# Performance work log

Measured on AMD Instinct MI355X. Metric: run time of the kernel, lower is better.

## Reference

```python
import jax, jax.numpy as jnp
import numpy as np

B, Q, C, H, N, D, F = 1, 2048, 2048, 1024, 16, 64, 4096
R = Q + C  # relative position encoding length
EPS = 1e-12
NEG = 1e30


def setup_inputs() -> dict:
    key = jax.random.key(0)
    ks = jax.random.split(key, 16)
    s = 0.02
    return dict(
        content_stream=jax.random.normal(ks[0], (B, Q, H), jnp.float32),
        content_mask=jnp.zeros((B, 1, Q, C), jnp.float32),
        context=jax.random.normal(ks[1], (B, C, H), jnp.float32),
        position_encoding=jax.random.normal(ks[2], (B, R, H), jnp.float32),
        content_bias=jax.random.normal(ks[3], (N, D), jnp.float32) * s,
        position_bias=jax.random.normal(ks[4], (N, D), jnp.float32) * s,
        segment_encoding=jax.random.normal(ks[5], (2, N, D), jnp.float32) * s,
        segment_matrix=jax.random.randint(ks[6], (B, Q, C), 0, 2).astype(bool),
        segment_bias=jax.random.normal(ks[7], (N, D), jnp.float32) * s,
        Wq=jax.random.normal(ks[8], (H, N, D), jnp.float32) * s,
        Wk=jax.random.normal(ks[9], (H, N, D), jnp.float32) * s,
        Wv=jax.random.normal(ks[10], (H, N, D), jnp.float32) * s,
        Wr=jax.random.normal(ks[11], (H, N, D), jnp.float32) * s,
        Wo=jax.random.normal(ks[12], (H, N, D), jnp.float32) * s,
        ln1_gamma=jnp.ones((H,), jnp.float32),
        ln1_beta=jnp.zeros((H,), jnp.float32),
        W1=jax.random.normal(ks[13], (H, F), jnp.float32) * s,
        b1=jnp.zeros((F,), jnp.float32),
        W2=jax.random.normal(ks[14], (F, H), jnp.float32) * s,
        b2=jnp.zeros((H,), jnp.float32),
        ln2_gamma=jnp.ones((H,), jnp.float32),
        ln2_beta=jnp.zeros((H,), jnp.float32),
    )


def _layernorm(x, g, b):
    m = jnp.mean(x, axis=-1, keepdims=True)
    v = jnp.mean(jnp.square(x - m), axis=-1, keepdims=True)
    return (x - m) * jax.lax.rsqrt(v + EPS) * g + b


def _rel_shift(x, klen):
    # x: [b, n, q, r] -> shifted [b, n, q, klen] (XLNet reshape trick)
    b, n, q, r = x.shape
    x = x.reshape(b, n, r, q)[:, :, 1:, :].reshape(b, n, q, r - 1)
    return x[:, :, :, :klen]


def reference(content_stream, content_mask, context, position_encoding,
              content_bias, position_bias, segment_encoding, segment_matrix,
              segment_bias, Wq, Wk, Wv, Wr, Wo, ln1_gamma, ln1_beta,
              W1, b1, W2, b2, ln2_gamma, ln2_beta):
    q = jnp.einsum('bqh,hnd->bqnd', content_stream, Wq)
    k = jnp.einsum('bch,hnd->bcnd', context, Wk)
    v = jnp.einsum('bch,hnd->bcnd', context, Wv)
    r = jnp.einsum('brh,hnd->brnd', position_encoding, Wr)

    # content / position / segment bias terms (XLNet relative attention)
    ac = jnp.einsum('bqnd,bcnd->bnqc', q + content_bias, k)
    bd = _rel_shift(jnp.einsum('bqnd,brnd->bnqr', q + position_bias, r),
                    k.shape[1])
    ef = jnp.einsum('bqnd,snd->bnqs', q + segment_bias, segment_encoding)
    ef = jnp.where(segment_matrix[:, None], ef[..., 1:], ef[..., :1])

    scores = (ac + bd + ef) / jnp.sqrt(jnp.float32(D))
    scores = scores - NEG * content_mask  # mask: 1.0 = disallowed
    probs = jax.nn.softmax(scores, axis=-1)

    attn = jnp.einsum('bnqc,bcnd->bqnd', probs, v)
    attn_out = jnp.einsum('bqnd,hnd->bqh', attn, Wo)

    # residual + LN, then FFN, residual + LN (dropout off: training=False)
    ffn_in = _layernorm(attn_out + content_stream, ln1_gamma, ln1_beta)
    ffn_out = jax.nn.relu(ffn_in @ W1 + b1) @ W2 + b2
    return _layernorm(ffn_out + ffn_in, ln2_gamma, ln2_beta)
```

## Files before the change

### kernel.cpp

```cpp
#include <hip/hip_runtime.h>
#include <stdint.h>


typedef unsigned short ushort_t;
typedef __attribute__((ext_vector_type(8))) short bf16x8;
typedef __attribute__((ext_vector_type(4))) float f32x4;

#define QLEN 2048
#define CLEN 2048
#define HDIM 1024
#define NHEAD 16
#define DHEAD 64
#define RLEN 4096
#define FDIM 4096

__device__ __forceinline__ float bf2f(ushort_t u) {
  union { float f; uint32_t i; } x; x.i = ((uint32_t)u) << 16; return x.f;
}
__device__ __forceinline__ ushort_t f2bf(float f) {
  union { float f; uint32_t i; } x; x.f = f;
  uint32_t r = x.i + 0x7fffu + ((x.i >> 16) & 1u);
  return (ushort_t)(r >> 16);
}
__device__ __forceinline__ f32x4 mfma16(bf16x8 a, bf16x8 b, f32x4 c) {
  return __builtin_amdgcn_mfma_f32_16x16x32_bf16(a, b, c, 0, 0, 0);
}
__device__ __forceinline__ bool probe_bf16(const uint32_t* probe) {
  return probe[0] == 0x3F803F80u;
}

typedef const __attribute__((address_space(1))) void* gas_t;
typedef __attribute__((address_space(3))) void* las_t;
__device__ __forceinline__ void glds16(const void* g, void* l) {
  __builtin_amdgcn_global_load_lds((gas_t)(uintptr_t)g, (las_t)(uintptr_t)l, 16, 0, 0);
}

__device__ __forceinline__ void bar_lds() {
  __asm__ volatile("s_waitcnt lgkmcnt(0)\n\ts_barrier" ::: "memory");
}
__device__ __forceinline__ void bar_full() {
  __asm__ volatile("s_waitcnt vmcnt(0) lgkmcnt(0)\n\ts_barrier" ::: "memory");
}

struct ConvJobs {
  const void* src[5];
  const void* mask_src;
  ushort_t* dst[5];
  int n[5];
  int blk0[6];
};

__global__ __launch_bounds__(256) void conv_all(
    ConvJobs J, const uint32_t* __restrict__ probe)
{
  const bool isb = probe_bf16(probe);
  int j = 0;
  #pragma unroll
  for (int t = 1; t < 5; t++) if ((int)blockIdx.x >= J.blk0[t]) j = t;
  const int lb = blockIdx.x - J.blk0[j];
  const int nb = J.blk0[j + 1] - J.blk0[j];
  const int n = J.n[j];
  ushort_t* dst = J.dst[j];
  if (j < 4) {
    const void* src = J.src[j];
    for (int i = lb * 256 + threadIdx.x; i < n; i += nb * 256)
      dst[i] = isb ? ((const ushort_t*)src)[i] : f2bf(((const float*)src)[i]);
  } else {
    const void* sm = J.src[4];
    uint32_t sw = 0;
    #pragma unroll
    for (int t = 0; t < 8; t++) sw |= ((const uint32_t*)sm)[t];
    const bool i8 = sw > 1u;
    for (int i = lb * 256 + threadIdx.x; i < n; i += nb * 256) {
      const int s = i8 ? (int)((const unsigned char*)sm)[i]
                       : (int)((const uint32_t*)sm)[i];
      const float mv = isb ? bf2f(((const ushort_t*)J.mask_src)[i])
                           : ((const float*)J.mask_src)[i];
      const float f = (float)(s ? 1 : 0) + (mv != 0.f ? 2.f : 0.f);
      dst[i] = f2bf(f);
    }
  }
}

struct SmallBatch {
  const void* src[10];
  int n[10];
  int off[10];
};

__global__ __launch_bounds__(256) void convert_small(
    SmallBatch sb, ushort_t* __restrict__ dst, const uint32_t* __restrict__ probe)
{
  const bool isb = probe_bf16(probe);
  const int t = blockIdx.x;
  const void* s = sb.src[t];
  ushort_t* d = dst + sb.off[t];
  for (int i = threadIdx.x; i < sb.n[t]; i += 256)
    d[i] = isb ? ((const ushort_t*)s)[i] : f2bf(((const float*)s)[i]);
}

struct TransJobs { const void* src[4]; ushort_t* dst[4]; };
__global__ __launch_bounds__(256) void transpose4_to_bf16(
    TransJobs T, int R, int C, const uint32_t* __restrict__ probe)
{
  const bool isb = probe_bf16(probe);
  const void* in = T.src[blockIdx.z];
  ushort_t* out = T.dst[blockIdx.z];
  __shared__ ushort_t t[32][33];
  const int bx = blockIdx.x * 32, by = blockIdx.y * 32;
  const int x = threadIdx.x & 31, y0 = threadIdx.x >> 5;
  #pragma unroll
  for (int yy = 0; yy < 32; yy += 8) {
    const size_t idx = (size_t)(by + y0 + yy) * C + bx + x;
    t[y0 + yy][x] = isb ? ((const ushort_t*)in)[idx] : f2bf(((const float*)in)[idx]);
  }
  __syncthreads();
  #pragma unroll
  for (int yy = 0; yy < 32; yy += 8)
    out[(size_t)(bx + y0 + yy) * R + by + x] = t[x][y0 + yy];
}

__global__ __launch_bounds__(256) void transpose_to_bf16(
    const void* __restrict__ in, ushort_t* __restrict__ out, int R, int C,
    const uint32_t* __restrict__ probe)
{
  const bool isb = probe_bf16(probe);
  __shared__ ushort_t t[32][33];
  const int bx = blockIdx.x * 32, by = blockIdx.y * 32;
  const int x = threadIdx.x & 31, y0 = threadIdx.x >> 5;
  #pragma unroll
  for (int yy = 0; yy < 32; yy += 8) {
    const size_t idx = (size_t)(by + y0 + yy) * C + bx + x;
    t[y0 + yy][x] = isb ? ((const ushort_t*)in)[idx] : f2bf(((const float*)in)[idx]);
  }
  __syncthreads();
  #pragma unroll
  for (int yy = 0; yy < 32; yy += 8)
    out[(size_t)(bx + y0 + yy) * R + by + x] = t[x][y0 + yy];
}

__device__ __forceinline__ void gemm_store(
    void* out, const ushort_t* bias, int M, int N, int epi,
    int gm, int gn, float v)
{
  if (epi == 0) {
    ((ushort_t*)out)[(size_t)gm * N + gn] = f2bf(v);
  } else if (epi == 1) {
    ((ushort_t*)out)[(size_t)gn * M + gm] = f2bf(v);
  } else if (epi == 2) {
    ((float*)out)[(size_t)gm * N + gn] = v;
  } else if (epi == 3) {
    v += bf2f(bias[gn]); v = v > 0.f ? v : 0.f;
    ((ushort_t*)out)[(size_t)gm * N + gn] = f2bf(v);
  } else if (epi == 4) {
    v += bf2f(bias[gn]);
    ((float*)out)[(size_t)gm * N + gn] = v;
  } else if (epi == 5) {
    ((ushort_t*)out)[((size_t)(gn >> 6) * M + gm) * 64 + (gn & 63)] = f2bf(v);
  } else {
    if (gn < 1024)
      ((ushort_t*)out)[((size_t)(gn >> 6) * M + gm) * 64 + (gn & 63)] = f2bf(v);
    else
      ((ushort_t*)out)[(size_t)2097152 + (size_t)(gn - 1024) * M + gm] = f2bf(v);
  }
}

__global__ __launch_bounds__(256) void gemm_bt_kernel(
    const ushort_t* __restrict__ A, const ushort_t* __restrict__ Bt,
    const ushort_t* __restrict__ bias, void* __restrict__ out,
    int M, int N, int K, int epi)
{
  __shared__ __attribute__((aligned(16))) ushort_t As[2][128 * 32];
  __shared__ __attribute__((aligned(16))) ushort_t Bs[2][64 * 32];
  const int tid = threadIdx.x;
  const int lane = tid & 63, wave = tid >> 6;
  const int l15 = lane & 15, quad = lane >> 4;
  const int m0 = blockIdx.y * 128, n0 = blockIdx.x * 64;

  const int arow = tid >> 2;
  const int acol = (tid & 3) * 8;

  f32x4 acc[2][4];
  #pragma unroll
  for (int i = 0; i < 2; i++)
    #pragma unroll
    for (int j = 0; j < 4; j++) acc[i][j] = (f32x4){0.f, 0.f, 0.f, 0.f};

  const int KI = K >> 5;
  glds16(&A[(size_t)(m0 + arow) * K + acol], &As[0][tid * 8]);
  glds16(&A[(size_t)(m0 + arow + 64) * K + acol], &As[0][tid * 8 + 2048]);
  glds16(&Bt[(size_t)(n0 + arow) * K + acol], &Bs[0][tid * 8]);
  bar_full();

  for (int ki = 0; ki < KI; ki++) {
    const int b = ki & 1;
    if (ki + 1 < KI) {
      const int k1 = (ki + 1) << 5;
      glds16(&A[(size_t)(m0 + arow) * K + k1 + acol], &As[b ^ 1][tid * 8]);
      glds16(&A[(size_t)(m0 + arow + 64) * K + k1 + acol], &As[b ^ 1][tid * 8 + 2048]);
      glds16(&Bt[(size_t)(n0 + arow) * K + k1 + acol], &Bs[b ^ 1][tid * 8]);
    }
    bf16x8 af[2], bfr[4];
    #pragma unroll
    for (int i = 0; i < 2; i++)
      af[i] = *(const bf16x8*)&As[b][(wave * 32 + i * 16 + l15) * 32 + quad * 8];
    #pragma unroll
    for (int j = 0; j < 4; j++)
      bfr[j] = *(const bf16x8*)&Bs[b][(j * 16 + l15) * 32 + quad * 8];
    #pragma unroll
    for (int i = 0; i < 2; i++)
      #pragma unroll
      for (int j = 0; j < 4; j++)
        acc[i][j] = mfma16(af[i], bfr[j], acc[i][j]);
    bar_full();
  }

  #pragma unroll
  for (int i = 0; i < 2; i++)
    #pragma unroll
    for (int j = 0; j < 4; j++)
      #pragma unroll
      for (int rg = 0; rg < 4; rg++)
        gemm_store(out, bias, M, N, epi,
                   m0 + wave * 32 + i * 16 + quad * 4 + rg,
                   n0 + j * 16 + l15, acc[i][j][rg]);
}

struct Ptr4 { void* p[4]; };
__global__ __launch_bounds__(256) void gemm128_bt_kernel(
    const ushort_t* __restrict__ A, const ushort_t* __restrict__ Bt,
    const ushort_t* __restrict__ bias, Ptr4 outs,
    int M, int N, int K, int Kc, int epi)
{
  __shared__ __attribute__((aligned(16))) ushort_t As[2][128 * 32];
  __shared__ __attribute__((aligned(16))) ushort_t Bs[2][128 * 32];
  const int tid = threadIdx.x;
  const int lane = tid & 63, wave = tid >> 6;
  const int l15 = lane & 15, quad = lane >> 4;
  const int wm = wave >> 1, wn = wave & 1;
  const int m0 = blockIdx.y * 128, n0 = blockIdx.x * 128;
  const int kb = blockIdx.z * Kc;
  void* out = outs.p[blockIdx.z];

  const int arow = tid >> 2;
  const int acol = (tid & 3) * 8;

  f32x4 acc[4][4];
  #pragma unroll
  for (int i = 0; i < 4; i++)
    #pragma unroll
    for (int j = 0; j < 4; j++) acc[i][j] = (f32x4){0.f, 0.f, 0.f, 0.f};

  const int KI = Kc >> 5;
  glds16(&A[(size_t)(m0 + arow) * K + kb + acol], &As[0][tid * 8]);
  glds16(&A[(size_t)(m0 + arow + 64) * K + kb + acol], &As[0][tid * 8 + 2048]);
  glds16(&Bt[(size_t)(n0 + arow) * K + kb + acol], &Bs[0][tid * 8]);
  glds16(&Bt[(size_t)(n0 + arow + 64) * K + kb + acol], &Bs[0][tid * 8 + 2048]);
  bar_full();

  for (int ki = 0; ki < KI; ki++) {
    const int b = ki & 1;
    if (ki + 1 < KI) {
      const int k1 = kb + ((ki + 1) << 5);
      glds16(&A[(size_t)(m0 + arow) * K + k1 + acol], &As[b ^ 1][tid * 8]);
      glds16(&A[(size_t)(m0 + arow + 64) * K + k1 + acol], &As[b ^ 1][tid * 8 + 2048]);
      glds16(&Bt[(size_t)(n0 + arow) * K + k1 + acol], &Bs[b ^ 1][tid * 8]);
      glds16(&Bt[(size_t)(n0 + arow + 64) * K + k1 + acol], &Bs[b ^ 1][tid * 8 + 2048]);
    }
    bf16x8 af[4], bfr[4];
    #pragma unroll
    for (int i = 0; i < 4; i++)
      af[i] = *(const bf16x8*)&As[b][(wm * 64 + i * 16 + l15) * 32 + quad * 8];
    #pragma unroll
    for (int j = 0; j < 4; j++)
      bfr[j] = *(const bf16x8*)&Bs[b][(wn * 64 + j * 16 + l15) * 32 + quad * 8];
    #pragma unroll
    for (int i = 0; i < 4; i++)
      #pragma unroll
      for (int j = 0; j < 4; j++)
        acc[i][j] = mfma16(af[i], bfr[j], acc[i][j]);
    bar_full();
  }

  #pragma unroll
  for (int i = 0; i < 4; i++)
    #pragma unroll
    for (int j = 0; j < 4; j++)
      #pragma unroll
      for (int rg = 0; rg < 4; rg++)
        gemm_store(out, bias, M, N, epi,
                   m0 + wm * 64 + i * 16 + quad * 4 + rg,
                   n0 + wn * 64 + j * 16 + l15, acc[i][j][rg]);
}

__global__ __launch_bounds__(256) void gemm64_bt_kernel(
    const ushort_t* __restrict__ A, const ushort_t* __restrict__ Bt,
    const ushort_t* __restrict__ bias, void* __restrict__ out,
    int M, int N, int K, int epi)
{
  __shared__ __attribute__((aligned(16))) ushort_t As[2][64 * 32];
  __shared__ __attribute__((aligned(16))) ushort_t Bs[2][64 * 32];
  const int tid = threadIdx.x;
  const int lane = tid & 63, wave = tid >> 6;
  const int l15 = lane & 15, quad = lane >> 4;
  const int wm = wave >> 1, wn = wave & 1;
  const int m0 = blockIdx.y * 64, n0 = blockIdx.x * 64;

  const int arow = tid >> 2;
  const int acol = (tid & 3) * 8;

  f32x4 acc[2][2];
  #pragma unroll
  for (int i = 0; i < 2; i++)
    #pragma unroll
    for (int j = 0; j < 2; j++) acc[i][j] = (f32x4){0.f, 0.f, 0.f, 0.f};

  const int KI = K >> 5;
  glds16(&A[(size_t)(m0 + arow) * K + acol], &As[0][tid * 8]);
  glds16(&Bt[(size_t)(n0 + arow) * K + acol], &Bs[0][tid * 8]);
  bar_full();

  for (int ki = 0; ki < KI; ki++) {
    const int b = ki & 1;
    if (ki + 1 < KI) {
      const int k1 = (ki + 1) << 5;
      glds16(&A[(size_t)(m0 + arow) * K + k1 + acol], &As[b ^ 1][tid * 8]);
      glds16(&Bt[(size_t)(n0 + arow) * K + k1 + acol], &Bs[b ^ 1][tid * 8]);
    }
    bf16x8 af[2], bfr[2];
    #pragma unroll
    for (int i = 0; i < 2; i++)
      af[i] = *(const bf16x8*)&As[b][(wm * 32 + i * 16 + l15) * 32 + quad * 8];
    #pragma unroll
    for (int j = 0; j < 2; j++)
      bfr[j] = *(const bf16x8*)&Bs[b][(wn * 32 + j * 16 + l15) * 32 + quad * 8];
    #pragma unroll
    for (int i = 0; i < 2; i++)
      #pragma unroll
      for (int j = 0; j < 2; j++)
        acc[i][j] = mfma16(af[i], bfr[j], acc[i][j]);
    bar_full();
  }

  #pragma unroll
  for (int i = 0; i < 2; i++)
    #pragma unroll
    for (int j = 0; j < 2; j++)
      #pragma unroll
      for (int rg = 0; rg < 4; rg++)
        gemm_store(out, bias, M, N, epi,
                   m0 + wm * 32 + i * 16 + quad * 4 + rg,
                   n0 + wn * 32 + j * 16 + l15, acc[i][j][rg]);
}

#define ESTR 36
#define PSTR2 72
__global__ __launch_bounds__(256, 2) void attn_flash(
    const ushort_t* __restrict__ qh, const ushort_t* __restrict__ kh,
    const ushort_t* __restrict__ vT, const ushort_t* __restrict__ rh,
    const ushort_t* __restrict__ cbias, const ushort_t* __restrict__ pbias,
    const ushort_t* __restrict__ sbias, const ushort_t* __restrict__ senc,
    const ushort_t* __restrict__ fmb, ushort_t* __restrict__ attn)
{
  __shared__ __attribute__((aligned(16))) ushort_t kbuf[2][64 * 64];
  __shared__ __attribute__((aligned(16))) ushort_t vbuf[2][64 * 64];
  __shared__ __attribute__((aligned(16))) ushort_t rbuf[2][80 * 64];
  __shared__ __attribute__((aligned(16))) ushort_t Pbuf[16 * PSTR2];
  __shared__ __attribute__((aligned(16))) float escr[4][16 * ESTR];
  __shared__ __attribute__((aligned(16))) ushort_t qpc[16 * 64];
  __shared__ __attribute__((aligned(16))) ushort_t qpp[16 * 64];
  __shared__ float wsum[4][16];
  __shared__ float e0s[16], e1s[16];

  const int n = blockIdx.x;
  const int q0 = blockIdx.y * 16;
  const int tid = threadIdx.x;
  const int lane = tid & 63, wave = tid >> 6;
  const int l15 = lane & 15, quad = lane >> 4;

  const ushort_t* qn = qh + (size_t)n * QLEN * 64;
  const ushort_t* kn = kh + (size_t)n * CLEN * 64;
  const ushort_t* rn = rh + (size_t)n * RLEN * 64;
  const ushort_t* vn = vT + (size_t)n * 64 * CLEN;

  const int srow = lane >> 3;
  const int sg = (lane & 7) ^ srow;

  for (int idx = tid; idx < 16 * 64; idx += 256) {
    const int row = idx >> 6, col = idx & 63;
    const float qv = bf2f(qn[(size_t)(q0 + row) * 64 + col]);
    qpc[idx] = f2bf(qv + bf2f(cbias[n * DHEAD + col]));
    qpp[idx] = f2bf(qv + bf2f(pbias[n * DHEAD + col]));
  }
  if (tid < 32) {
    const int row = tid & 15, sidx = tid >> 4;
    float a = 0.f;
    for (int d = 0; d < DHEAD; d++)
      a += (bf2f(qn[(size_t)(q0 + row) * 64 + d]) + bf2f(sbias[n * DHEAD + d]))
           * bf2f(senc[(size_t)(sidx * NHEAD + n) * DHEAD + d]);
    if (sidx == 0) e0s[row] = a; else e1s[row] = a;
  }

  {
    const int c0 = 0, ua = c0 - q0 + (QLEN - 16);
    if (wave == 0) {
      #pragma unroll
      for (int i = 0; i < 8; i++)
        glds16(kn + (size_t)(c0 + i * 8 + srow) * 64 + sg * 8, &kbuf[0][i * 512]);
    } else if (wave == 1) {
      #pragma unroll
      for (int i = 0; i < 8; i++)
        glds16(vn + (size_t)(i * 8 + srow) * CLEN + c0 + sg * 8, &vbuf[0][i * 512]);
    } else if (wave == 2) {
      #pragma unroll
      for (int i = 0; i < 8; i++)
        glds16(rn + (size_t)(ua + i * 8 + srow) * 64 + sg * 8, &rbuf[0][i * 512]);
    } else {
      #pragma unroll
      for (int i = 0; i < 2; i++)
        glds16(rn + (size_t)(ua + 64 + i * 8 + srow) * 64 + sg * 8, &rbuf[0][(64 + i * 8) * 64]);
    }
  }
  bar_full();

  const bf16x8* qpc8 = (const bf16x8*)qpc;
  const bf16x8* qpp8 = (const bf16x8*)qpp;
  const bf16x8 qc0 = qpc8[l15 * 8 + quad];
  const bf16x8 qc1 = qpc8[l15 * 8 + 4 + quad];
  const bf16x8 qp0 = qpp8[l15 * 8 + quad];
  const bf16x8 qp1 = qpp8[l15 * 8 + 4 + quad];
  const float a0_ = e0s[l15] * 0.125f;
  const float ad_ = (e1s[l15] - e0s[l15]) * 0.125f;

  float* escr_w = escr[wave];
  const int gk0 = quad ^ (l15 & 7);
  const int gk1 = (quad + 4) ^ (l15 & 7);

  float l_row = 0.f;
  f32x4 O = (f32x4){0.f, 0.f, 0.f, 0.f};

  const size_t eoff_base = (size_t)(q0 + l15) * CLEN + wave * 16 + quad * 4;

  for (int ci = 0; ci < CLEN / 64; ci++) {
    const int b = ci & 1;

    const uint2 fmv = *(const uint2*)&fmb[eoff_base + (size_t)ci * 64];

    if (ci + 1 < CLEN / 64) {
      const int c1 = (ci + 1) * 64, ua1 = c1 - q0 + (QLEN - 16);
      if (wave == 0) {
        #pragma unroll
        for (int i = 0; i < 8; i++)
          glds16(kn + (size_t)(c1 + i * 8 + srow) * 64 + sg * 8, &kbuf[b ^ 1][i * 512]);
      } else if (wave == 1) {
        #pragma unroll
        for (int i = 0; i < 8; i++)
          glds16(vn + (size_t)(i * 8 + srow) * CLEN + c1 + sg * 8, &vbuf[b ^ 1][i * 512]);
      } else if (wave == 2) {
        #pragma unroll
        for (int i = 0; i < 8; i++)
          glds16(rn + (size_t)(ua1 + i * 8 + srow) * 64 + sg * 8, &rbuf[b ^ 1][i * 512]);
      } else {
        #pragma unroll
        for (int i = 0; i < 2; i++)
          glds16(rn + (size_t)(ua1 + 64 + i * 8 + srow) * 64 + sg * 8, &rbuf[b ^ 1][(64 + i * 8) * 64]);
      }
    }

    #pragma unroll
    for (int t = 0; t < 2; t++) {
      const int rrow = (wave + t) * 16 + l15;
      f32x4 e = (f32x4){0.f, 0.f, 0.f, 0.f};
      e = mfma16(*(const bf16x8*)&rbuf[b][rrow * 64 + gk0 * 8], qp0, e);
      e = mfma16(*(const bf16x8*)&rbuf[b][rrow * 64 + gk1 * 8], qp1, e);
      *(f32x4*)&escr_w[l15 * ESTR + t * 16 + quad * 4] = e;
    }

    const int krow = wave * 16 + l15;
    f32x4 a = (f32x4){0.f, 0.f, 0.f, 0.f};
    a = mfma16(*(const bf16x8*)&kbuf[b][krow * 64 + gk0 * 8], qc0, a);
    a = mfma16(*(const bf16x8*)&kbuf[b][krow * 64 + gk1 * 8], qc1, a);

    const ushort_t fm4[4] = {(ushort_t)(fmv.x & 0xffff), (ushort_t)(fmv.x >> 16),
                             (ushort_t)(fmv.y & 0xffff), (ushort_t)(fmv.y >> 16)};
    const float* dg = &escr_w[l15 * ESTR + quad * 4 - l15 + 16];
    float p[4], psum = 0.f;
    #pragma unroll
    for (int rg = 0; rg < 4; rg++) {
      const float f = bf2f(fm4[rg]);
      const float mk = floorf(f * 0.5f);
      const float sm = f - 2.f * mk;
      float v = fmaf(a[rg] + dg[rg], 0.125f, fmaf(sm, ad_, a0_));
      v = fmaf(mk, -1.0e30f, v);
      p[rg] = __expf(v);
      psum += p[rg];
    }
    psum += __shfl_xor(psum, 16);
    psum += __shfl_xor(psum, 32);
    l_row += psum;

    {
      uint2 pk;
      pk.x = (uint32_t)f2bf(p[0]) | ((uint32_t)f2bf(p[1]) << 16);
      pk.y = (uint32_t)f2bf(p[2]) | ((uint32_t)f2bf(p[3]) << 16);
      *(uint2*)&Pbuf[l15 * PSTR2 + wave * 16 + quad * 4] = pk;
    }
    bar_lds();

    const bf16x8 pa0 = *(const bf16x8*)&Pbuf[l15 * PSTR2 + quad * 8];
    const bf16x8 pa1 = *(const bf16x8*)&Pbuf[l15 * PSTR2 + 32 + quad * 8];
    const int vrow = wave * 16 + l15;
    O = mfma16(pa0, *(const bf16x8*)&vbuf[b][vrow * 64 + gk0 * 8], O);
    O = mfma16(pa1, *(const bf16x8*)&vbuf[b][vrow * 64 + gk1 * 8], O);

    bar_full();
  }

  if (quad == 0) wsum[wave][l15] = l_row;
  __syncthreads();
  const float l = wsum[0][l15] + wsum[1][l15] + wsum[2][l15] + wsum[3][l15];
  const float linv = 1.0f / l;
  float linv4[4];
  #pragma unroll
  for (int rg = 0; rg < 4; rg++) linv4[rg] = __shfl(linv, quad * 4 + rg);
  #pragma unroll
  for (int rg = 0; rg < 4; rg++)
    attn[(size_t)(q0 + quad * 4 + rg) * HDIM + n * 64 + wave * 16 + l15] =
        f2bf(O[rg] * linv4[rg]);
}

__global__ __launch_bounds__(256) void ln_kernel(
    const float* __restrict__ x0, const float* __restrict__ x1,
    const float* __restrict__ x2, const float* __restrict__ x3,
    const ushort_t* __restrict__ res_bf, const float* __restrict__ res_f,
    const ushort_t* __restrict__ badd,
    const ushort_t* __restrict__ gamma, const ushort_t* __restrict__ beta,
    ushort_t* __restrict__ out_bf, float* __restrict__ out_f,
    void* __restrict__ out_dyn, const uint32_t* __restrict__ probe)
{
  const int row = blockIdx.x, tid = threadIdx.x;
  const int lane = tid & 63, wave = tid >> 6;
  __shared__ float red[8];
  const size_t base = (size_t)row * HDIM;
  float v[4];
  #pragma unroll
  for (int i = 0; i < 4; i++) {
    const int h = tid + i * 256;
    float xv = x0[base + h];
    if (x1) xv += x1[base + h] + x2[base + h] + x3[base + h];
    if (badd) xv += bf2f(badd[h]);
    const float rv = res_bf ? bf2f(res_bf[base + h]) : res_f[base + h];
    v[i] = xv + rv;
  }
  float s = v[0] + v[1] + v[2] + v[3];
  float ss = v[0] * v[0] + v[1] * v[1] + v[2] * v[2] + v[3] * v[3];
  #pragma unroll
  for (int off = 32; off > 0; off >>= 1) {
    s += __shfl_xor(s, off);
    ss += __shfl_xor(ss, off);
  }
  if (lane == 0) { red[wave] = s; red[4 + wave] = ss; }
  __syncthreads();
  s = red[0] + red[1] + red[2] + red[3];
  ss = red[4] + red[5] + red[6] + red[7];
  const float mean = s * (1.0f / HDIM);
  float var = ss * (1.0f / HDIM) - mean * mean;
  var = var > 0.f ? var : 0.f;
  const float rs = rsqrtf(var + 1e-12f);
  const bool outb = out_dyn ? probe_bf16(probe) : false;
  #pragma unroll
  for (int i = 0; i < 4; i++) {
    const int h = tid + i * 256;
    const float y = (v[i] - mean) * rs * bf2f(gamma[h]) + bf2f(beta[h]);
    if (out_bf) out_bf[base + h] = f2bf(y);
    if (out_f)  out_f[base + h] = y;
    if (out_dyn) {
      if (outb) ((ushort_t*)out_dyn)[base + h] = f2bf(y);
      else      ((float*)out_dyn)[base + h] = y;
    }
  }
}

extern "C" void kernel_launch(void* const* d_in, const int* in_sizes, int n_in,
                              void* d_out, int out_size, void* d_ws, size_t ws_size,
                              hipStream_t stream)
{
  (void)in_sizes; (void)n_in; (void)out_size; (void)ws_size;

  const void* cs_r   = d_in[0];
  const void* mask_r = d_in[1];
  const void* ctx_r  = d_in[2];
  const void* pe_r   = d_in[3];
  const void* cb_r   = d_in[4];
  const void* pb_r   = d_in[5];
  const void* senc_r = d_in[6];
  const void* smat   = d_in[7];
  const void* sb_r   = d_in[8];
  const void* Wq_r   = d_in[9];
  const void* Wk_r   = d_in[10];
  const void* Wv_r   = d_in[11];
  const void* Wr_r   = d_in[12];
  const void* Wo_r   = d_in[13];
  const void* g1_r   = d_in[14];
  const void* be1_r  = d_in[15];
  const void* W1_r   = d_in[16];
  const void* b1_r   = d_in[17];
  const void* W2_r   = d_in[18];
  const void* b2_r   = d_in[19];
  const void* g2_r   = d_in[20];
  const void* be2_r  = d_in[21];

  const uint32_t* probe = (const uint32_t*)g1_r;

  char* w = (char*)d_ws;
  #define WSOFF(mb) ((void*)(w + ((size_t)(mb) << 20)))
  ushort_t* fm_b     = (ushort_t*)WSOFF(0);
  ushort_t* Wqt      = (ushort_t*)WSOFF(8);
  ushort_t* Wkt      = (ushort_t*)WSOFF(10);
  ushort_t* Wvt      = (ushort_t*)WSOFF(12);
  ushort_t* Wrt      = (ushort_t*)WSOFF(14);
  ushort_t* W1t      = (ushort_t*)WSOFF(16);
  ushort_t* W2t      = (ushort_t*)WSOFF(24);
  ushort_t* Wo_b     = (ushort_t*)WSOFF(32);
  ushort_t* smalls   = (ushort_t*)WSOFF(34);
  ushort_t* cs_b     = (ushort_t*)WSOFF(35);
  ushort_t* ctx_b    = (ushort_t*)WSOFF(47);
  ushort_t* pe_b     = (ushort_t*)WSOFF(51);
  ushort_t* qbuf     = (ushort_t*)WSOFF(59);
  ushort_t* kbuf     = (ushort_t*)WSOFF(63);
  ushort_t* vTbuf    = (ushort_t*)WSOFF(67);
  ushort_t* rbuf     = (ushort_t*)WSOFF(71);
  ushort_t* attnbuf  = (ushort_t*)WSOFF(79);
  float*    attn_out = (float*)WSOFF(83);
  ushort_t* ffn_in_b = (ushort_t*)WSOFF(91);
  ushort_t* hidden   = (ushort_t*)WSOFF(39);
  float*    ffn_in_f = (float*)WSOFF(71);
  float*    fp0      = (float*)WSOFF(0);
  float*    fp1      = (float*)WSOFF(8);
  float*    fp2      = (float*)WSOFF(59);
  float*    fp3      = (float*)WSOFF(83);

  ushort_t* cb   = smalls + 0;
  ushort_t* pb   = smalls + 1024;
  ushort_t* sb   = smalls + 2048;
  ushort_t* senc = smalls + 3072;
  ushort_t* b1   = smalls + 5120;
  ushort_t* b2   = smalls + 9216;
  ushort_t* g1   = smalls + 10240;
  ushort_t* be1  = smalls + 11264;
  ushort_t* g2   = smalls + 12288;
  ushort_t* be2  = smalls + 13312;

  const dim3 blk(256);

  SmallBatch sbatch;
  const void* ssrc[10] = {cb_r, pb_r, sb_r, senc_r, b1_r, b2_r, g1_r, be1_r, g2_r, be2_r};
  const int   sn[10]   = {1024, 1024, 1024, 2048, 4096, 1024, 1024, 1024, 1024, 1024};
  const int   soff[10] = {0, 1024, 2048, 3072, 5120, 9216, 10240, 11264, 12288, 13312};
  for (int i = 0; i < 10; i++) { sbatch.src[i] = ssrc[i]; sbatch.n[i] = sn[i]; sbatch.off[i] = soff[i]; }
  convert_small<<<10, blk, 0, stream>>>(sbatch, smalls, probe);

  ConvJobs cj;
  cj.src[0] = cs_r;  cj.dst[0] = cs_b;  cj.n[0] = QLEN * HDIM;
  cj.src[1] = ctx_r; cj.dst[1] = ctx_b; cj.n[1] = CLEN * HDIM;
  cj.src[2] = pe_r;  cj.dst[2] = pe_b;  cj.n[2] = RLEN * HDIM;
  cj.src[3] = Wo_r;  cj.dst[3] = Wo_b;  cj.n[3] = HDIM * HDIM;
  cj.src[4] = smat;  cj.dst[4] = fm_b;  cj.n[4] = QLEN * CLEN;
  cj.mask_src = mask_r;
  int pfx = 0;
  for (int i = 0; i < 5; i++) {
    cj.blk0[i] = pfx;
    pfx += (cj.n[i] + 2047) / 2048;
  }
  cj.blk0[5] = pfx;
  conv_all<<<pfx, blk, 0, stream>>>(cj, probe);

  TransJobs tj;
  tj.src[0] = Wq_r; tj.dst[0] = Wqt;
  tj.src[1] = Wk_r; tj.dst[1] = Wkt;
  tj.src[2] = Wv_r; tj.dst[2] = Wvt;
  tj.src[3] = Wr_r; tj.dst[3] = Wrt;
  transpose4_to_bf16<<<dim3(32, 32, 4), blk, 0, stream>>>(tj, HDIM, HDIM, probe);
  transpose_to_bf16<<<dim3(128, 32), blk, 0, stream>>>(W1_r, W1t, HDIM, FDIM, probe);
  transpose_to_bf16<<<dim3(32, 128), blk, 0, stream>>>(W2_r, W2t, FDIM, HDIM, probe);

  gemm64_bt_kernel<<<dim3(16, 32), blk, 0, stream>>>(cs_b,  Wqt, nullptr, qbuf,  QLEN, HDIM, HDIM, 5);
  gemm_bt_kernel<<<dim3(32, 16), blk, 0, stream>>>(ctx_b, Wkt, nullptr, kbuf, CLEN, 2048, HDIM, 6);
  gemm_bt_kernel<<<dim3(16, 32), blk, 0, stream>>>(pe_b,  Wrt, nullptr, rbuf,  RLEN, HDIM, HDIM, 5);

  attn_flash<<<dim3(NHEAD, QLEN / 16), blk, 0, stream>>>(
      qbuf, kbuf, vTbuf, rbuf, cb, pb, sb, senc, fm_b, attnbuf);

  gemm64_bt_kernel<<<dim3(16, 32), blk, 0, stream>>>(attnbuf, Wo_b, nullptr, attn_out, QLEN, HDIM, HDIM, 2);

  ln_kernel<<<QLEN, blk, 0, stream>>>(attn_out, nullptr, nullptr, nullptr,
                                      cs_b, nullptr, nullptr, g1, be1,
                                      ffn_in_b, ffn_in_f, nullptr, probe);

  Ptr4 o1; o1.p[0] = hidden; o1.p[1] = o1.p[2] = o1.p[3] = nullptr;
  gemm128_bt_kernel<<<dim3(32, 16, 1), blk, 0, stream>>>(
      ffn_in_b, W1t, b1, o1, QLEN, FDIM, HDIM, HDIM, 3);

  Ptr4 o2; o2.p[0] = fp0; o2.p[1] = fp1; o2.p[2] = fp2; o2.p[3] = fp3;
  gemm128_bt_kernel<<<dim3(8, 16, 4), blk, 0, stream>>>(
      hidden, W2t, nullptr, o2, QLEN, HDIM, FDIM, FDIM / 4, 2);

  ln_kernel<<<QLEN, blk, 0, stream>>>(fp0, fp1, fp2, fp3,
                                      nullptr, ffn_in_f, b2, g2, be2,
                                      nullptr, nullptr, d_out, probe);
  #undef WSOFF
}
```

Measured before the change: 533.0 us.

## Process 32 query rows per attention block to reuse K/V/R tiles

The flash attention kernel now handles 32 query rows per block instead of 16, so each loaded K, V and relative-position tile is used for two 16-row MMA groups. The K and V fragments are loaded once from LDS and applied to both halves. The q-plus-bias staging buffers now share the score scratch area, and the R tile grows to 96 rows to cover the wider shift window. This halves global K/V/R traffic and barrier count per query row, at the cost of more registers per thread and half as many blocks.

```diff
diff --git a/kernel.cpp b/kernel.cpp
--- a/kernel.cpp
+++ b/kernel.cpp
@@ -364,16 +364,14 @@
 {
   __shared__ __attribute__((aligned(16))) ushort_t kbuf[2][64 * 64];
   __shared__ __attribute__((aligned(16))) ushort_t vbuf[2][64 * 64];
-  __shared__ __attribute__((aligned(16))) ushort_t rbuf[2][80 * 64];
-  __shared__ __attribute__((aligned(16))) ushort_t Pbuf[16 * PSTR2];
-  __shared__ __attribute__((aligned(16))) float escr[4][16 * ESTR];
-  __shared__ __attribute__((aligned(16))) ushort_t qpc[16 * 64];
-  __shared__ __attribute__((aligned(16))) ushort_t qpp[16 * 64];
-  __shared__ float wsum[4][16];
-  __shared__ float e0s[16], e1s[16];
+  __shared__ __attribute__((aligned(16))) ushort_t rbuf[2][96 * 64];
+  __shared__ __attribute__((aligned(16))) ushort_t Pbuf[32 * PSTR2];
+  __shared__ __attribute__((aligned(16))) float escr[4 * 16 * ESTR];
+  __shared__ float wsum[4][32];
+  __shared__ float e0s[32], e1s[32];
 
   const int n = blockIdx.x;
-  const int q0 = blockIdx.y * 16;
+  const int q0 = blockIdx.y * 32;
   const int tid = threadIdx.x;
   const int lane = tid & 63, wave = tid >> 6;
   const int l15 = lane & 15, quad = lane >> 4;
@@ -386,23 +384,37 @@
   const int srow = lane >> 3;
   const int sg = (lane & 7) ^ srow;
 
-  for (int idx = tid; idx < 16 * 64; idx += 256) {
+  ushort_t* qpcS = (ushort_t*)escr;
+  ushort_t* qppS = qpcS + 32 * 64;
+  for (int idx = tid; idx < 32 * 64; idx += 256) {
     const int row = idx >> 6, col = idx & 63;
     const float qv = bf2f(qn[(size_t)(q0 + row) * 64 + col]);
-    qpc[idx] = f2bf(qv + bf2f(cbias[n * DHEAD + col]));
-    qpp[idx] = f2bf(qv + bf2f(pbias[n * DHEAD + col]));
-  }
-  if (tid < 32) {
-    const int row = tid & 15, sidx = tid >> 4;
+    qpcS[idx] = f2bf(qv + bf2f(cbias[n * DHEAD + col]));
+    qppS[idx] = f2bf(qv + bf2f(pbias[n * DHEAD + col]));
+  }
+  if (wave == 3) {
+    const int row = lane & 31, sidx = lane >> 5;
     float a = 0.f;
     for (int d = 0; d < DHEAD; d++)
       a += (bf2f(qn[(size_t)(q0 + row) * 64 + d]) + bf2f(sbias[n * DHEAD + d]))
            * bf2f(senc[(size_t)(sidx * NHEAD + n) * DHEAD + d]);
     if (sidx == 0) e0s[row] = a; else e1s[row] = a;
   }
+  __syncthreads();
+
+  const bf16x8* qpc8 = (const bf16x8*)qpcS;
+  const bf16x8* qpp8 = (const bf16x8*)qppS;
+  bf16x8 qcf[2][2], qpf[2][2];
+  #pragma unroll
+  for (int hq = 0; hq < 2; hq++)
+    #pragma unroll
+    for (int h = 0; h < 2; h++) {
+      qcf[hq][h] = qpc8[(hq * 16 + l15) * 8 + h * 4 + quad];
+      qpf[hq][h] = qpp8[(hq * 16 + l15) * 8 + h * 4 + quad];
+    }
 
   {
-    const int c0 = 0, ua = c0 - q0 + (QLEN - 16);
+    const int c0 = 0, ua = c0 - q0 + (QLEN - 32);
     if (wave == 0) {
       #pragma unroll
       for (int i = 0; i < 8; i++)
@@ -417,37 +429,41 @@
         glds16(rn + (size_t)(ua + i * 8 + srow) * 64 + sg * 8, &rbuf[0][i * 512]);
     } else {
       #pragma unroll
-      for (int i = 0; i < 2; i++)
+      for (int i = 0; i < 4; i++)
         glds16(rn + (size_t)(ua + 64 + i * 8 + srow) * 64 + sg * 8, &rbuf[0][(64 + i * 8) * 64]);
     }
   }
   bar_full();
 
-  const bf16x8* qpc8 = (const bf16x8*)qpc;
-  const bf16x8* qpp8 = (const bf16x8*)qpp;
-  const bf16x8 qc0 = qpc8[l15 * 8 + quad];
-  const bf16x8 qc1 = qpc8[l15 * 8 + 4 + quad];
-  const bf16x8 qp0 = qpp8[l15 * 8 + quad];
-  const bf16x8 qp1 = qpp8[l15 * 8 + 4 + quad];
-  const float a0_ = e0s[l15] * 0.125f;
-  const float ad_ = (e1s[l15] - e0s[l15]) * 0.125f;
-
-  float* escr_w = escr[wave];
+  float a0q[2], adq[2];
+  #pragma unroll
+  for (int hq = 0; hq < 2; hq++) {
+    const float e0 = e0s[hq * 16 + l15], e1 = e1s[hq * 16 + l15];
+    a0q[hq] = e0 * 0.125f;
+    adq[hq] = (e1 - e0) * 0.125f;
+  }
+
+  float* escr_w = escr + wave * (16 * ESTR);
   const int gk0 = quad ^ (l15 & 7);
   const int gk1 = (quad + 4) ^ (l15 & 7);
 
-  float l_row = 0.f;
-  f32x4 O = (f32x4){0.f, 0.f, 0.f, 0.f};
-
-  const size_t eoff_base = (size_t)(q0 + l15) * CLEN + wave * 16 + quad * 4;
+  float l_row[2] = {0.f, 0.f};
+  f32x4 O[2];
+  O[0] = (f32x4){0.f, 0.f, 0.f, 0.f};
+  O[1] = (f32x4){0.f, 0.f, 0.f, 0.f};
+
+  const size_t eo0 = (size_t)(q0 + l15) * CLEN + wave * 16 + quad * 4;
+  const size_t eo1 = eo0 + (size_t)16 * CLEN;
 
   for (int ci = 0; ci < CLEN / 64; ci++) {
     const int b = ci & 1;
 
-    const uint2 fmv = *(const uint2*)&fmb[eoff_base + (size_t)ci * 64];
+    uint2 fmv[2];
+    fmv[0] = *(const uint2*)&fmb[eo0 + (size_t)ci * 64];
+    fmv[1] = *(const uint2*)&fmb[eo1 + (size_t)ci * 64];
 
     if (ci + 1 < CLEN / 64) {
-      const int c1 = (ci + 1) * 64, ua1 = c1 - q0 + (QLEN - 16);
+      const int c1 = (ci + 1) * 64, ua1 = c1 - q0 + (QLEN - 32);
       if (wave == 0) {
         #pragma unroll
         for (int i = 0; i < 8; i++)
@@ -462,71 +478,85 @@
           glds16(rn + (size_t)(ua1 + i * 8 + srow) * 64 + sg * 8, &rbuf[b ^ 1][i * 512]);
       } else {
         #pragma unroll
-        for (int i = 0; i < 2; i++)
+        for (int i = 0; i < 4; i++)
           glds16(rn + (size_t)(ua1 + 64 + i * 8 + srow) * 64 + sg * 8, &rbuf[b ^ 1][(64 + i * 8) * 64]);
       }
     }
 
-    #pragma unroll
-    for (int t = 0; t < 2; t++) {
-      const int rrow = (wave + t) * 16 + l15;
-      f32x4 e = (f32x4){0.f, 0.f, 0.f, 0.f};
-      e = mfma16(*(const bf16x8*)&rbuf[b][rrow * 64 + gk0 * 8], qp0, e);
-      e = mfma16(*(const bf16x8*)&rbuf[b][rrow * 64 + gk1 * 8], qp1, e);
-      *(f32x4*)&escr_w[l15 * ESTR + t * 16 + quad * 4] = e;
-    }
-
     const int krow = wave * 16 + l15;
-    f32x4 a = (f32x4){0.f, 0.f, 0.f, 0.f};
-    a = mfma16(*(const bf16x8*)&kbuf[b][krow * 64 + gk0 * 8], qc0, a);
-    a = mfma16(*(const bf16x8*)&kbuf[b][krow * 64 + gk1 * 8], qc1, a);
-
-    const ushort_t fm4[4] = {(ushort_t)(fmv.x & 0xffff), (ushort_t)(fmv.x >> 16),
-                             (ushort_t)(fmv.y & 0xffff), (ushort_t)(fmv.y >> 16)};
-    const float* dg = &escr_w[l15 * ESTR + quad * 4 - l15 + 16];
-    float p[4], psum = 0.f;
-    #pragma unroll
-    for (int rg = 0; rg < 4; rg++) {
-      const float f = bf2f(fm4[rg]);
-      const float mk = floorf(f * 0.5f);
-      const float sm = f - 2.f * mk;
-      float v = fmaf(a[rg] + dg[rg], 0.125f, fmaf(sm, ad_, a0_));
-      v = fmaf(mk, -1.0e30f, v);
-      p[rg] = __expf(v);
-      psum += p[rg];
-    }
-    psum += __shfl_xor(psum, 16);
-    psum += __shfl_xor(psum, 32);
-    l_row += psum;
-
-    {
+    const bf16x8 kf0 = *(const bf16x8*)&kbuf[b][krow * 64 + gk0 * 8];
+    const bf16x8 kf1 = *(const bf16x8*)&kbuf[b][krow * 64 + gk1 * 8];
+
+    #pragma unroll
+    for (int hq = 0; hq < 2; hq++) {
+      #pragma unroll
+      for (int t = 0; t < 2; t++) {
+        const int rrow = wave * 16 + ((1 - hq) + t) * 16 + l15;
+        f32x4 e = (f32x4){0.f, 0.f, 0.f, 0.f};
+        e = mfma16(*(const bf16x8*)&rbuf[b][rrow * 64 + gk0 * 8], qpf[hq][0], e);
+        e = mfma16(*(const bf16x8*)&rbuf[b][rrow * 64 + gk1 * 8], qpf[hq][1], e);
+        *(f32x4*)&escr_w[l15 * ESTR + t * 16 + quad * 4] = e;
+      }
+
+      f32x4 a = (f32x4){0.f, 0.f, 0.f, 0.f};
+      a = mfma16(kf0, qcf[hq][0], a);
+      a = mfma16(kf1, qcf[hq][1], a);
+
+      const uint2 fv = fmv[hq];
+      const ushort_t fm4[4] = {(ushort_t)(fv.x & 0xffff), (ushort_t)(fv.x >> 16),
+                               (ushort_t)(fv.y & 0xffff), (ushort_t)(fv.y >> 16)};
+      const float* dg = &escr_w[l15 * ESTR + quad * 4 - l15 + 16];
+      float p[4], psum = 0.f;
+      #pragma unroll
+      for (int rg = 0; rg < 4; rg++) {
+        const float f = bf2f(fm4[rg]);
+        const float mk = floorf(f * 0.5f);
+        const float sm = f - 2.f * mk;
+        float v = fmaf(a[rg] + dg[rg], 0.125f, fmaf(sm, adq[hq], a0q[hq]));
+        v = fmaf(mk, -1.0e30f, v);
+        p[rg] = __expf(v);
+        psum += p[rg];
+      }
+      psum += __shfl_xor(psum, 16);
+      psum += __shfl_xor(psum, 32);
+      l_row[hq] += psum;
+
       uint2 pk;
       pk.x = (uint32_t)f2bf(p[0]) | ((uint32_t)f2bf(p[1]) << 16);
       pk.y = (uint32_t)f2bf(p[2]) | ((uint32_t)f2bf(p[3]) << 16);
-      *(uint2*)&Pbuf[l15 * PSTR2 + wave * 16 + quad * 4] = pk;
+      *(uint2*)&Pbuf[(hq * 16 + l15) * PSTR2 + wave * 16 + quad * 4] = pk;
     }
     bar_lds();
 
-    const bf16x8 pa0 = *(const bf16x8*)&Pbuf[l15 * PSTR2 + quad * 8];
-    const bf16x8 pa1 = *(const bf16x8*)&Pbuf[l15 * PSTR2 + 32 + quad * 8];
     const int vrow = wave * 16 + l15;
-    O = mfma16(pa0, *(const bf16x8*)&vbuf[b][vrow * 64 + gk0 * 8], O);
-    O = mfma16(pa1, *(const bf16x8*)&vbuf[b][vrow * 64 + gk1 * 8], O);
+    const bf16x8 vf0 = *(const bf16x8*)&vbuf[b][vrow * 64 + gk0 * 8];
+    const bf16x8 vf1 = *(const bf16x8*)&vbuf[b][vrow * 64 + gk1 * 8];
+    #pragma unroll
+    for (int hq = 0; hq < 2; hq++) {
+      const bf16x8 pa0 = *(const bf16x8*)&Pbuf[(hq * 16 + l15) * PSTR2 + quad * 8];
+      const bf16x8 pa1 = *(const bf16x8*)&Pbuf[(hq * 16 + l15) * PSTR2 + 32 + quad * 8];
+      O[hq] = mfma16(pa0, vf0, O[hq]);
+      O[hq] = mfma16(pa1, vf1, O[hq]);
+    }
 
     bar_full();
   }
 
-  if (quad == 0) wsum[wave][l15] = l_row;
+  if (quad == 0) { wsum[wave][l15] = l_row[0]; wsum[wave][16 + l15] = l_row[1]; }
   __syncthreads();
-  const float l = wsum[0][l15] + wsum[1][l15] + wsum[2][l15] + wsum[3][l15];
-  const float linv = 1.0f / l;
-  float linv4[4];
-  #pragma unroll
-  for (int rg = 0; rg < 4; rg++) linv4[rg] = __shfl(linv, quad * 4 + rg);
-  #pragma unroll
-  for (int rg = 0; rg < 4; rg++)
-    attn[(size_t)(q0 + quad * 4 + rg) * HDIM + n * 64 + wave * 16 + l15] =
-        f2bf(O[rg] * linv4[rg]);
+  #pragma unroll
+  for (int hq = 0; hq < 2; hq++) {
+    const int qi = hq * 16 + l15;
+    const float l = wsum[0][qi] + wsum[1][qi] + wsum[2][qi] + wsum[3][qi];
+    const float linv = 1.0f / l;
+    float linv4[4];
+    #pragma unroll
+    for (int rg = 0; rg < 4; rg++) linv4[rg] = __shfl(linv, quad * 4 + rg);
+    #pragma unroll
+    for (int rg = 0; rg < 4; rg++)
+      attn[(size_t)(q0 + hq * 16 + quad * 4 + rg) * HDIM + n * 64 + wave * 16 + l15] =
+          f2bf(O[hq][rg] * linv4[rg]);
+  }
 }
 
 __global__ __launch_bounds__(256) void ln_kernel(
@@ -688,7 +718,7 @@
   gemm_bt_kernel<<<dim3(32, 16), blk, 0, stream>>>(ctx_b, Wkt, nullptr, kbuf, CLEN, 2048, HDIM, 6);
   gemm_bt_kernel<<<dim3(16, 32), blk, 0, stream>>>(pe_b,  Wrt, nullptr, rbuf,  RLEN, HDIM, HDIM, 5);
 
-  attn_flash<<<dim3(NHEAD, QLEN / 16), blk, 0, stream>>>(
+  attn_flash<<<dim3(NHEAD, QLEN / 32), blk, 0, stream>>>(
       qbuf, kbuf, vTbuf, rbuf, cb, pb, sb, senc, fm_b, attnbuf);
 
   gemm64_bt_kernel<<<dim3(16, 32), blk, 0, stream>>>(attnbuf, Wo_b, nullptr, attn_out, QLEN, HDIM, HDIM, 2);
```

New measurement: 489.8 us. -8.1%, faster.
